# Kernel tuning notes

Hardware: AMD Instinct MI355X
Metric: run time of the kernel (lower is better)

The kernel has to match this reference:

```python
import jax, jax.numpy as jnp
import numpy as np
import math

N = 4096
BATCH = 8192


def _bitrev_perm(n):
    stages = int(math.log2(n))
    idx = np.arange(n, dtype=np.int64)
    rev = np.zeros(n, dtype=np.int64)
    v = idx.copy()
    for _ in range(stages):
        rev = (rev << 1) | (v & 1)
        v >>= 1
    return rev


def setup_inputs() -> dict:
    key = jax.random.key(0)
    k1, k2 = jax.random.split(key)
    x_re = jax.random.normal(k1, (BATCH, N), dtype=jnp.float32)
    x_im = jax.random.normal(k2, (BATCH, N), dtype=jnp.float32)
    k = np.arange(N, dtype=np.float32)
    angles = -2.0 * np.pi * k / N
    W_re = jnp.asarray(np.cos(angles), dtype=jnp.float32)
    W_im = jnp.asarray(np.sin(angles), dtype=jnp.float32)
    bitrev = jnp.asarray(_bitrev_perm(N))
    return {"x_re": x_re, "x_im": x_im, "W_re": W_re, "W_im": W_im, "bitrev": bitrev}


def reference(x_re, x_im, W_re, W_im, bitrev):
    n = x_re.shape[-1]
    num_stages = int(math.log2(n))
    # bit-reversal input permutation (the "wiring")
    y_re = x_re[..., bitrev]
    y_im = x_im[..., bitrev]
    for stage in range(num_stages):
        stride = 1 << stage
        group_size = stride << 1
        num_groups = n // group_size
        # (..., num_groups, group_size)
        y_re = y_re.reshape(*y_re.shape[:-1], num_groups, group_size)
        y_im = y_im.reshape(*y_im.shape[:-1], num_groups, group_size)
        upper_re = y_re[..., :stride]
        upper_im = y_im[..., :stride]
        lower_re = y_re[..., stride:]
        lower_im = y_im[..., stride:]
        tw_step = n // group_size
        tw_idx = jnp.arange(stride) * tw_step
        Wr = W_re[tw_idx]
        Wi = W_im[tw_idx]
        # complex twiddle multiply: W * lower
        wb_re = Wr * lower_re - Wi * lower_im
        wb_im = Wr * lower_im + Wi * lower_re
        y_re = jnp.concatenate([upper_re + wb_re, upper_re - wb_re], axis=-1)
        y_im = jnp.concatenate([upper_im + wb_im, upper_im - wb_im], axis=-1)
        y_re = y_re.reshape(*y_re.shape[:-2], n)
        y_im = y_im.reshape(*y_im.shape[:-2], n)
    return (y_re, y_im)
```

## Files before the change

### kernel.cpp

```cpp
#include <hip/hip_runtime.h>

#define FFT_N   4096
#define THREADS 256

__device__ __forceinline__ float2 cmul(float2 w, float2 v) {
    return make_float2(fmaf(w.x, v.x, -w.y * v.y), fmaf(w.x, v.y, w.y * v.x));
}
__device__ __forceinline__ float2 cmni(float2 v) { return make_float2(v.y, -v.x); }
__device__ __forceinline__ void bfly(float2& a, float2& b, float2 w) {
    float2 t = cmul(w, b);
    b = make_float2(a.x - t.x, a.y - t.y);
    a = make_float2(a.x + t.x, a.y + t.y);
}
__device__ __forceinline__ void bfly1(float2& a, float2& b) {
    float2 t = b;
    b = make_float2(a.x - t.x, a.y - t.y);
    a = make_float2(a.x + t.x, a.y + t.y);
}
__device__ __forceinline__ void bflyni(float2& a, float2& b) {
    float2 t = make_float2(b.y, -b.x);
    b = make_float2(a.x - t.x, a.y - t.y);
    a = make_float2(a.x + t.x, a.y + t.y);
}
__device__ __forceinline__ int swz(int i) { return i ^ ((i >> 4) & 15) ^ ((i >> 8) & 15); }
__device__ __forceinline__ void bar() {
    asm volatile("s_waitcnt lgkmcnt(0)" ::: "memory");
    __builtin_amdgcn_s_barrier();
}

#define Q1x  0.70710678118654752f
#define Q3x -0.70710678118654752f
#define E1x 0.923879532511286756f
#define E1y -0.382683432365089772f
#define E3x 0.382683432365089772f
#define E3y -0.923879532511286756f

__device__ __forceinline__ void radix16(float2 u[16], float2 G, float2 G2, float2 G4, float2 G8) {
#pragma unroll
    for (int m = 0; m < 16; m += 2) bfly(u[m], u[m + 1], G8);
    float2 G4n = cmni(G4);
#pragma unroll
    for (int b = 0; b < 16; b += 4) { bfly(u[b], u[b + 2], G4); bfly(u[b + 1], u[b + 3], G4n); }
    float2 t1 = cmul(G2, make_float2(Q1x, -Q1x));
    float2 t2 = cmni(G2);
    float2 t3 = cmul(G2, make_float2(Q3x, -Q1x));
#pragma unroll
    for (int b = 0; b < 16; b += 8) {
        bfly(u[b + 0], u[b + 4], G2); bfly(u[b + 1], u[b + 5], t1);
        bfly(u[b + 2], u[b + 6], t2); bfly(u[b + 3], u[b + 7], t3);
    }
    float2 s1 = cmul(G, make_float2(E1x, E1y));
    float2 s2 = cmul(G, make_float2(Q1x, -Q1x));
    float2 s3 = cmul(G, make_float2(E3x, E3y));
    float2 s4 = cmni(G);
    float2 s5 = cmni(s1);
    float2 s6 = cmni(s2);
    float2 s7 = cmni(s3);
    bfly(u[0], u[8],  G);  bfly(u[1], u[9],  s1);
    bfly(u[2], u[10], s2); bfly(u[3], u[11], s3);
    bfly(u[4], u[12], s4); bfly(u[5], u[13], s5);
    bfly(u[6], u[14], s6); bfly(u[7], u[15], s7);
}

__device__ __forceinline__ void radix16_first(float2 u[16]) {
#pragma unroll
    for (int m = 0; m < 16; m += 2) bfly1(u[m], u[m + 1]);
#pragma unroll
    for (int b = 0; b < 16; b += 4) { bfly1(u[b], u[b + 2]); bflyni(u[b + 1], u[b + 3]); }
#pragma unroll
    for (int b = 0; b < 16; b += 8) {
        bfly1(u[b + 0], u[b + 4]);
        bfly(u[b + 1], u[b + 5], make_float2(Q1x, -Q1x));
        bflyni(u[b + 2], u[b + 6]);
        bfly(u[b + 3], u[b + 7], make_float2(Q3x, -Q1x));
    }
    bfly1(u[0], u[8]);
    bfly(u[1], u[9],  make_float2(E1x, E1y));
    bfly(u[2], u[10], make_float2(Q1x, -Q1x));
    bfly(u[3], u[11], make_float2(E3x, E3y));
    bflyni(u[4], u[12]);
    bfly(u[5], u[13], make_float2(E1y, -E1x));
    bfly(u[6], u[14], make_float2(Q3x, -Q1x));
    bfly(u[7], u[15], make_float2(E3y, -E3x));
}

__global__ __launch_bounds__(THREADS) void fft4096_r16_kernel(
    const float* __restrict__ x_re, const float* __restrict__ x_im,
    const float* __restrict__ W_re, const float* __restrict__ W_im,
    float* __restrict__ out, int batch, int rows_per)
{
    __shared__ float2 lds[FFT_N];
    const int t = threadIdx.x;

    const int rB = t & 15;
    const float2 GB  = make_float2(W_re[rB << 4], W_im[rB << 4]);
    const float2 GB2 = cmul(GB, GB);
    const float2 GB4 = cmul(GB2, GB2);
    const float2 GB8 = cmul(GB4, GB4);
    const float2 GC  = make_float2(W_re[t], W_im[t]);
    const float2 GC2 = cmul(GC, GC);
    const float2 GC4 = cmul(GC2, GC2);
    const float2 GC8 = cmul(GC4, GC4);

    const int g  = (int)(__brev((unsigned)t) >> 24);
    const int bB = (t & 15) | ((t >> 4) << 8);
    const int row0 = blockIdx.x * rows_per;
    float* out_im = out + (size_t)batch * FFT_N;

    for (int i = 0; i < rows_per; ++i) {
        const int r = row0 + i;
        const float* xr = x_re + (size_t)r * FFT_N;
        const float* xi = x_im + (size_t)r * FFT_N;
        float2 u[16];

        const int off[16] = {0, 2048, 1024, 3072, 512, 2560, 1536, 3584,
                             256, 2304, 1280, 3328, 768, 2816, 1792, 3840};
#pragma unroll
        for (int j = 0; j < 16; ++j) u[j] = make_float2(xr[t + off[j]], xi[t + off[j]]);

        radix16_first(u);
#pragma unroll
        for (int j = 0; j < 16; ++j) lds[swz(16 * g + j)] = u[j];
        bar();

#pragma unroll
        for (int j = 0; j < 16; ++j) u[j] = lds[swz(bB + 16 * j)];
        radix16(u, GB, GB2, GB4, GB8);
#pragma unroll
        for (int j = 0; j < 16; ++j) lds[swz(bB + 16 * j)] = u[j];
        bar();

#pragma unroll
        for (int j = 0; j < 16; ++j) u[j] = lds[swz(t + 256 * j)];
        radix16(u, GC, GC2, GC4, GC8);
        float* yr = out + (size_t)r * FFT_N;
        float* yi = out_im + (size_t)r * FFT_N;
#pragma unroll
        for (int j = 0; j < 16; ++j) { yr[t + 256 * j] = u[j].x; yi[t + 256 * j] = u[j].y; }
        bar();
    }
}

extern "C" void kernel_launch(void* const* d_in, const int* in_sizes, int n_in,
                              void* d_out, int out_size, void* d_ws, size_t ws_size,
                              hipStream_t stream) {
    const float* x_re = (const float*)d_in[0];
    const float* x_im = (const float*)d_in[1];
    const float* W_re = (const float*)d_in[2];
    const float* W_im = (const float*)d_in[3];
    const int batch = in_sizes[0] / FFT_N;
    float* out = (float*)d_out;

    int rows_per = 8;
    while (rows_per > 1 && (batch % rows_per)) rows_per >>= 1;
    const int grid = batch / rows_per;
    fft4096_r16_kernel<<<grid, THREADS, 0, stream>>>(x_re, x_im, W_re, W_im, out, batch, rows_per);
}
```

Before: 123.6 us.

## Software-pipeline next-row global loads across FFT stages with register double buffering

Restructures the per-block row loop so each thread prefetches the next row's 16 complex inputs into a second register buffer. The prefetch is split into chunks issued between the three radix-16 stages, so global-memory latency overlaps with LDS traffic and arithmetic. The cost is about 32 more live VGPRs per thread, which may lower occupancy or cause spills. Odd rows_per falls back to the unpipelined path.

```diff
diff --git a/kernel.cpp b/kernel.cpp
--- a/kernel.cpp
+++ b/kernel.cpp
@@ -84,7 +84,58 @@
     bfly(u[7], u[15], make_float2(E3y, -E3x));
 }
 
-__global__ __launch_bounds__(THREADS) void fft4096_r16_kernel(
+struct Row { float2 u[16]; };
+
+__device__ __constant__ const int koff[16] = {0, 2048, 1024, 3072, 512, 2560, 1536, 3584,
+                                              256, 2304, 1280, 3328, 768, 2816, 1792, 3840};
+
+__device__ __forceinline__ void load_row(Row& r, const float* __restrict__ xr,
+                                         const float* __restrict__ xi, int t) {
+#pragma unroll
+    for (int j = 0; j < 16; ++j) r.u[j] = make_float2(xr[t + koff[j]], xi[t + koff[j]]);
+}
+
+template <int J0, int CNT>
+__device__ __forceinline__ void issueN(Row& n, const float* __restrict__ xr,
+                                       const float* __restrict__ xi, int t, bool en) {
+    if (en) {
+#pragma unroll
+        for (int j = J0; j < J0 + CNT; ++j) n.u[j] = make_float2(xr[t + koff[j]], xi[t + koff[j]]);
+    }
+    asm volatile("" ::: "memory");
+}
+
+__device__ __forceinline__ void process_row(Row& W, Row& P, float2* lds, int t,
+        float2 GB, float2 GB2, float2 GB4, float2 GB8,
+        float2 GC, float2 GC2, float2 GC4, float2 GC8,
+        int g, int bB,
+        float* __restrict__ yr, float* __restrict__ yi,
+        const float* __restrict__ nxr, const float* __restrict__ nxi, bool more)
+{
+    issueN<0, 6>(P, nxr, nxi, t, more);
+    radix16_first(W.u);
+#pragma unroll
+    for (int j = 0; j < 16; ++j) lds[swz(16 * g + j)] = W.u[j];
+    bar();
+
+    issueN<6, 5>(P, nxr, nxi, t, more);
+#pragma unroll
+    for (int j = 0; j < 16; ++j) W.u[j] = lds[swz(bB + 16 * j)];
+    radix16(W.u, GB, GB2, GB4, GB8);
+#pragma unroll
+    for (int j = 0; j < 16; ++j) lds[swz(bB + 16 * j)] = W.u[j];
+    bar();
+
+    issueN<11, 5>(P, nxr, nxi, t, more);
+#pragma unroll
+    for (int j = 0; j < 16; ++j) W.u[j] = lds[swz(t + 256 * j)];
+    radix16(W.u, GC, GC2, GC4, GC8);
+#pragma unroll
+    for (int j = 0; j < 16; ++j) { yr[t + 256 * j] = W.u[j].x; yi[t + 256 * j] = W.u[j].y; }
+    bar();
+}
+
+__global__ __launch_bounds__(THREADS) void fft4096_r16p_kernel(
     const float* __restrict__ x_re, const float* __restrict__ x_im,
     const float* __restrict__ W_re, const float* __restrict__ W_im,
     float* __restrict__ out, int batch, int rows_per)
@@ -106,38 +157,34 @@
     const int bB = (t & 15) | ((t >> 4) << 8);
     const int row0 = blockIdx.x * rows_per;
     float* out_im = out + (size_t)batch * FFT_N;
-
-    for (int i = 0; i < rows_per; ++i) {
-        const int r = row0 + i;
-        const float* xr = x_re + (size_t)r * FFT_N;
-        const float* xi = x_im + (size_t)r * FFT_N;
-        float2 u[16];
-
-        const int off[16] = {0, 2048, 1024, 3072, 512, 2560, 1536, 3584,
-                             256, 2304, 1280, 3328, 768, 2816, 1792, 3840};
-#pragma unroll
-        for (int j = 0; j < 16; ++j) u[j] = make_float2(xr[t + off[j]], xi[t + off[j]]);
-
-        radix16_first(u);
-#pragma unroll
-        for (int j = 0; j < 16; ++j) lds[swz(16 * g + j)] = u[j];
-        bar();
-
-#pragma unroll
-        for (int j = 0; j < 16; ++j) u[j] = lds[swz(bB + 16 * j)];
-        radix16(u, GB, GB2, GB4, GB8);
-#pragma unroll
-        for (int j = 0; j < 16; ++j) lds[swz(bB + 16 * j)] = u[j];
-        bar();
-
-#pragma unroll
-        for (int j = 0; j < 16; ++j) u[j] = lds[swz(t + 256 * j)];
-        radix16(u, GC, GC2, GC4, GC8);
-        float* yr = out + (size_t)r * FFT_N;
-        float* yi = out_im + (size_t)r * FFT_N;
-#pragma unroll
-        for (int j = 0; j < 16; ++j) { yr[t + 256 * j] = u[j].x; yi[t + 256 * j] = u[j].y; }
-        bar();
+    Row X, Y;
+
+    if (rows_per & 1) {
+        for (int i = 0; i < rows_per; ++i) {
+            const int r = row0 + i;
+            load_row(X, x_re + (size_t)r * FFT_N, x_im + (size_t)r * FFT_N, t);
+            asm volatile("" ::: "memory");
+            process_row(X, Y, lds, t, GB, GB2, GB4, GB8, GC, GC2, GC4, GC8, g, bB,
+                        out + (size_t)r * FFT_N, out_im + (size_t)r * FFT_N,
+                        x_re, x_im, false);
+        }
+        return;
+    }
+
+    load_row(X, x_re + (size_t)row0 * FFT_N, x_im + (size_t)row0 * FFT_N, t);
+    asm volatile("" ::: "memory");
+
+    for (int i = 0; i < rows_per; i += 2) {
+        const int r0 = row0 + i, r1 = r0 + 1;
+        const bool m1 = (i + 2) < rows_per;
+        const int r2 = m1 ? (r0 + 2) : row0;
+
+        process_row(X, Y, lds, t, GB, GB2, GB4, GB8, GC, GC2, GC4, GC8, g, bB,
+                    out + (size_t)r0 * FFT_N, out_im + (size_t)r0 * FFT_N,
+                    x_re + (size_t)r1 * FFT_N, x_im + (size_t)r1 * FFT_N, true);
+        process_row(Y, X, lds, t, GB, GB2, GB4, GB8, GC, GC2, GC4, GC8, g, bB,
+                    out + (size_t)r1 * FFT_N, out_im + (size_t)r1 * FFT_N,
+                    x_re + (size_t)r2 * FFT_N, x_im + (size_t)r2 * FFT_N, m1);
     }
 }
 
@@ -154,5 +201,5 @@
     int rows_per = 8;
     while (rows_per > 1 && (batch % rows_per)) rows_per >>= 1;
     const int grid = batch / rows_per;
-    fft4096_r16_kernel<<<grid, THREADS, 0, stream>>>(x_re, x_im, W_re, W_im, out, batch, rows_per);
-}
+    fft4096_r16p_kernel<<<grid, THREADS, 0, stream>>>(x_re, x_im, W_re, W_im, out, batch, rows_per);
+}
```

New measurement: 118.0 us. -4.6%, faster.
